# Kernel tuning notes

Hardware: AMD Instinct MI355X
Metric: run time of the kernel (lower is better)

Reference implementation:

```python
import jax, jax.numpy as jnp
import numpy as np

EPS = 1e-5

def setup_inputs() -> dict:
    key = jax.random.key(0)
    ks = jax.random.split(key, 8)
    N, D = 65536, 256
    x = jax.random.normal(ks[0], (N, D), dtype=jnp.float32)
    # BatchNorm1d affine params (frozen, torch default init)
    bn_gamma = jnp.ones((D,), jnp.float32)
    bn_beta = jnp.zeros((D,), jnp.float32)
    # Linear layers, torch default uniform(-1/sqrt(fan_in), 1/sqrt(fan_in))
    def lin(k, fin, fout):
        k1, k2 = jax.random.split(k)
        bound = 1.0 / np.sqrt(fin)
        W = jax.random.uniform(k1, (fout, fin), jnp.float32, -bound, bound)
        b = jax.random.uniform(k2, (fout,), jnp.float32, -bound, bound)
        return W, b
    W1, b1 = lin(ks[1], D, 512)
    W2, b2 = lin(ks[2], 512, 2048)
    Wf, bf = lin(ks[3], 2048, D)
    return {"x": x, "bn_gamma": bn_gamma, "bn_beta": bn_beta,
            "W1": W1, "b1": b1, "W2": W2, "b2": b2, "Wf": Wf, "bf": bf}


def reference(x, bn_gamma, bn_beta, W1, b1, W2, b2, Wf, bf):
    # BatchNorm1d in training mode: per-batch mean / biased variance
    mu = jnp.mean(x, axis=0)
    var = jnp.mean(jnp.square(x - mu), axis=0)
    xn = (x - mu) * jax.lax.rsqrt(var + EPS) * bn_gamma + bn_beta
    raw_feats = jnp.tanh(xn)
    h = xn @ W1.T + b1          # [N, 512]
    h = h @ W2.T + b2           # [N, 2048]
    out = jnp.tanh(h @ Wf.T + bf)  # [N, latent_dim]
    return (out, raw_feats)
```

## Files before the change

kernel.cpp:

```cpp
#include <hip/hip_runtime.h>
#include <hip/hip_bf16.h>
#include <stdint.h>

#define NROWS 65536
#define DFEAT 256

typedef __bf16 bf16x8 __attribute__((ext_vector_type(8)));
typedef float f32x4 __attribute__((ext_vector_type(4)));

__device__ __forceinline__ float fast_tanh(float x) {
    return 1.0f - 2.0f / (__expf(2.0f * x) + 1.0f);
}

__device__ __forceinline__ void gload_lds16(const void* g, void* l) {
    __builtin_amdgcn_global_load_lds(
        (const __attribute__((address_space(1))) unsigned int*)g,
        (__attribute__((address_space(3))) unsigned int*)l, 16, 0, 0);
}

__global__ void stats_kernel(const float4* __restrict__ x4,
                             float* __restrict__ sums,
                             float* __restrict__ sumsq) {
    __shared__ float ps[4][256];
    __shared__ float pq[4][256];
    int t = threadIdx.x;
    int c4 = t & 63;
    int r  = t >> 6;
    size_t i0 = (size_t)blockIdx.x * 128;
    float4 s = make_float4(0.f, 0.f, 0.f, 0.f);
    float4 q = make_float4(0.f, 0.f, 0.f, 0.f);
    for (int i = r; i < 128; i += 4) {
        float4 v = x4[(i0 + i) * 64 + c4];
        s.x += v.x; s.y += v.y; s.z += v.z; s.w += v.w;
        q.x += v.x * v.x; q.y += v.y * v.y; q.z += v.z * v.z; q.w += v.w * v.w;
    }
    ps[r][c4 * 4 + 0] = s.x; ps[r][c4 * 4 + 1] = s.y;
    ps[r][c4 * 4 + 2] = s.z; ps[r][c4 * 4 + 3] = s.w;
    pq[r][c4 * 4 + 0] = q.x; pq[r][c4 * 4 + 1] = q.y;
    pq[r][c4 * 4 + 2] = q.z; pq[r][c4 * 4 + 3] = q.w;
    __syncthreads();
    float ts = ps[0][t] + ps[1][t] + ps[2][t] + ps[3][t];
    float tq = pq[0][t] + pq[1][t] + pq[2][t] + pq[3][t];
    atomicAdd(&sums[t], ts);
    atomicAdd(&sumsq[t], tq);
}

__global__ void finalize_mvu_kernel(const float* __restrict__ sums,
                                    const float* __restrict__ sumsq,
                                    const float* __restrict__ gamma,
                                    const float* __restrict__ beta,
                                    float* __restrict__ scl,
                                    float* __restrict__ sft,
                                    const float* __restrict__ W2,
                                    const float* __restrict__ b1,
                                    const float* __restrict__ b2,
                                    float* __restrict__ u) {
    int t = threadIdx.x;
    if (blockIdx.x == 0) {
        const float invN = 1.0f / (float)NROWS;
        float mu  = sums[t] * invN;
        float var = sumsq[t] * invN - mu * mu;
        float rs  = rsqrtf(var + 1e-5f);
        float a   = gamma[t] * rs;
        scl[t] = a;
        sft[t] = beta[t] - mu * a;
        return;
    }
    int lane = t & 63;
    int row = (blockIdx.x - 1) * 4 + (t >> 6);
    const float* Wr = W2 + (size_t)row * 512;
    float s = 0.f;
    for (int k = lane; k < 512; k += 64) s += Wr[k] * b1[k];
    #pragma unroll
    for (int off = 32; off; off >>= 1) s += __shfl_xor(s, off);
    if (lane == 0) u[row] = s + b2[row];
}

__global__ void pgemm_kernel(const float* __restrict__ A,
                             const float* __restrict__ B,
                             float* __restrict__ C) {
    __shared__ float As[32][33];
    __shared__ float Bs[32][33];
    int t = threadIdx.x;
    int tx = t & 15, ty = t >> 4;
    int bi = blockIdx.y * 32;
    int bj = blockIdx.x * 32;
    int kb = blockIdx.z * 512;
    int row = t >> 3;
    int col = (t & 7) * 4;
    float acc00 = 0.f, acc01 = 0.f, acc10 = 0.f, acc11 = 0.f;
    for (int k0 = kb; k0 < kb + 512; k0 += 32) {
        float4 av = *(const float4*)&A[(size_t)(bi + row) * 2048 + k0 + col];
        As[row][col + 0] = av.x; As[row][col + 1] = av.y;
        As[row][col + 2] = av.z; As[row][col + 3] = av.w;
        float4 bv = *(const float4*)&B[(size_t)(k0 + row) * 512 + bj + col];
        Bs[row][col + 0] = bv.x; Bs[row][col + 1] = bv.y;
        Bs[row][col + 2] = bv.z; Bs[row][col + 3] = bv.w;
        __syncthreads();
        #pragma unroll
        for (int k = 0; k < 32; ++k) {
            float a0 = As[ty * 2 + 0][k];
            float a1 = As[ty * 2 + 1][k];
            float b0 = Bs[k][tx * 2 + 0];
            float b1v = Bs[k][tx * 2 + 1];
            acc00 += a0 * b0; acc01 += a0 * b1v;
            acc10 += a1 * b0; acc11 += a1 * b1v;
        }
        __syncthreads();
    }
    int i = bi + ty * 2, j = bj + tx * 2;
    atomicAdd(&C[(size_t)(i + 0) * 512 + j + 0], acc00);
    atomicAdd(&C[(size_t)(i + 0) * 512 + j + 1], acc01);
    atomicAdd(&C[(size_t)(i + 1) * 512 + j + 0], acc10);
    atomicAdd(&C[(size_t)(i + 1) * 512 + j + 1], acc11);
}

__global__ void collapse2_kernel(const float* __restrict__ P,
                                 const float* __restrict__ W1,
                                 const float* __restrict__ Wf,
                                 const float* __restrict__ u,
                                 const float* __restrict__ bfv,
                                 __bf16* __restrict__ Bprep,
                                 float* __restrict__ cv) {
    __shared__ float As[32][33];
    __shared__ float Bs[32][33];
    int t = threadIdx.x;
    if (blockIdx.x >= 64) {
        int lane = t & 63;
        int row = (blockIdx.x - 64) * 4 + (t >> 6);
        const float* Wr = Wf + (size_t)row * 2048;
        float s = 0.f;
        for (int k = lane; k < 2048; k += 64) s += Wr[k] * u[k];
        #pragma unroll
        for (int off = 32; off; off >>= 1) s += __shfl_xor(s, off);
        if (lane == 0) cv[row] = s + bfv[row];
        return;
    }
    int tx = t & 15, ty = t >> 4;
    int bi = (blockIdx.x >> 3) * 32;
    int bj = (blockIdx.x & 7) * 32;
    int row = t >> 3;
    int col = (t & 7) * 4;
    float acc00 = 0.f, acc01 = 0.f, acc10 = 0.f, acc11 = 0.f;
    for (int k0 = 0; k0 < 512; k0 += 32) {
        float4 av = *(const float4*)&P[(size_t)(bi + row) * 512 + k0 + col];
        As[row][col + 0] = av.x; As[row][col + 1] = av.y;
        As[row][col + 2] = av.z; As[row][col + 3] = av.w;
        float4 bv = *(const float4*)&W1[(size_t)(k0 + row) * 256 + bj + col];
        Bs[row][col + 0] = bv.x; Bs[row][col + 1] = bv.y;
        Bs[row][col + 2] = bv.z; Bs[row][col + 3] = bv.w;
        __syncthreads();
        #pragma unroll
        for (int k = 0; k < 32; ++k) {
            float a0 = As[ty * 2 + 0][k];
            float a1 = As[ty * 2 + 1][k];
            float b0 = Bs[k][tx * 2 + 0];
            float b1v = Bs[k][tx * 2 + 1];
            acc00 += a0 * b0; acc01 += a0 * b1v;
            acc10 += a1 * b0; acc11 += a1 * b1v;
        }
        __syncthreads();
    }
    int j = bi + ty * 2, k = bj + tx * 2;
    float vals[2][2] = {{acc00, acc01}, {acc10, acc11}};
    #pragma unroll
    for (int dj = 0; dj < 2; ++dj)
        #pragma unroll
        for (int dk = 0; dk < 2; ++dk) {
            float v = vals[dj][dk];
            int jj = j + dj, kk = k + dk;
            __bf16 h = (__bf16)v;
            __bf16 lo = (__bf16)(v - (float)h);
            int kstep = kk >> 5, kgrp = (kk >> 3) & 3, e = kk & 7;
            Bprep[((((size_t)kstep * 2 + 0) * 4 + kgrp) * 256 + jj) * 8 + e] = h;
            Bprep[((((size_t)kstep * 2 + 1) * 4 + kgrp) * 256 + jj) * 8 + e] = lo;
        }
}

__global__ __launch_bounds__(256)
void main_mfma(const float4* __restrict__ x4,
               const float* __restrict__ scl,
               const float* __restrict__ sft,
               const __bf16* __restrict__ Bprep,
               const float* __restrict__ cvec,
               float* __restrict__ out,
               float4* __restrict__ rf4) {
    __shared__ __align__(16) __bf16 Abuf[2][4][64][8];
    __shared__ __align__(16) __bf16 Bbuf[2][4][256][8];
    __shared__ float ss[256], sh[256];
    int t = threadIdx.x;
    int l = t & 63;
    int w = t >> 6;
    ss[t] = scl[t];
    sh[t] = sft[t];
    size_t row0 = (size_t)blockIdx.x * 64;
    int arow = t >> 2;
    int akg  = t & 3;

    f32x4 acc[4][4];
    #pragma unroll
    for (int i = 0; i < 4; ++i)
        #pragma unroll
        for (int j = 0; j < 4; ++j)
            acc[i][j] = (f32x4){0.f, 0.f, 0.f, 0.f};
    __syncthreads();

    int g = l >> 4, li = l & 15;
    for (int s = 0; s < 8; ++s) {
        const __bf16* bsrc = Bprep + (size_t)s * 16384;
        __bf16* bdst = &Bbuf[0][0][0][0];
        #pragma unroll
        for (int c = 0; c < 8; ++c) {
            int slot = c * 256 + t;
            gload_lds16(bsrc + (size_t)slot * 8, bdst + (size_t)slot * 8);
        }
        size_t xbase = (row0 + arow) * 64 + s * 8 + akg * 2;
        float4 v0 = x4[xbase];
        float4 v1 = x4[xbase + 1];
        int kb = s * 32 + akg * 8;
        float xn[8];
        xn[0] = v0.x * ss[kb + 0] + sh[kb + 0];
        xn[1] = v0.y * ss[kb + 1] + sh[kb + 1];
        xn[2] = v0.z * ss[kb + 2] + sh[kb + 2];
        xn[3] = v0.w * ss[kb + 3] + sh[kb + 3];
        xn[4] = v1.x * ss[kb + 4] + sh[kb + 4];
        xn[5] = v1.y * ss[kb + 5] + sh[kb + 5];
        xn[6] = v1.z * ss[kb + 6] + sh[kb + 6];
        xn[7] = v1.w * ss[kb + 7] + sh[kb + 7];
        float4 r0, r1;
        r0.x = fast_tanh(xn[0]); r0.y = fast_tanh(xn[1]);
        r0.z = fast_tanh(xn[2]); r0.w = fast_tanh(xn[3]);
        r1.x = fast_tanh(xn[4]); r1.y = fast_tanh(xn[5]);
        r1.z = fast_tanh(xn[6]); r1.w = fast_tanh(xn[7]);
        rf4[xbase] = r0;
        rf4[xbase + 1] = r1;
        bf16x8 hv, lv;
        #pragma unroll
        for (int e = 0; e < 8; ++e) {
            __bf16 h = (__bf16)xn[e];
            hv[e] = h;
            lv[e] = (__bf16)(xn[e] - (float)h);
        }
        int rx = arow ^ (akg << 1);
        *(bf16x8*)&Abuf[0][akg][rx][0] = hv;
        *(bf16x8*)&Abuf[1][akg][rx][0] = lv;
        __syncthreads();

        bf16x8 ah[4], al[4];
        #pragma unroll
        for (int i = 0; i < 4; ++i) {
            int rxr = (i * 16 + li) ^ (g << 1);
            ah[i] = *(const bf16x8*)&Abuf[0][g][rxr][0];
            al[i] = *(const bf16x8*)&Abuf[1][g][rxr][0];
        }
        #pragma unroll
        for (int j = 0; j < 4; ++j) {
            int coll = w * 64 + j * 16 + li;
            bf16x8 bh = *(const bf16x8*)&Bbuf[0][g][coll][0];
            bf16x8 bl = *(const bf16x8*)&Bbuf[1][g][coll][0];
            #pragma unroll
            for (int i = 0; i < 4; ++i) {
                acc[i][j] = __builtin_amdgcn_mfma_f32_16x16x32_bf16(ah[i], bh, acc[i][j], 0, 0, 0);
                acc[i][j] = __builtin_amdgcn_mfma_f32_16x16x32_bf16(al[i], bh, acc[i][j], 0, 0, 0);
                acc[i][j] = __builtin_amdgcn_mfma_f32_16x16x32_bf16(ah[i], bl, acc[i][j], 0, 0, 0);
            }
        }
        __syncthreads();
    }

    #pragma unroll
    for (int j = 0; j < 4; ++j) {
        int gcol = w * 64 + j * 16 + li;
        float cj = cvec[gcol];
        #pragma unroll
        for (int i = 0; i < 4; ++i) {
            #pragma unroll
            for (int r = 0; r < 4; ++r) {
                size_t grow = row0 + i * 16 + g * 4 + r;
                out[grow * 256 + gcol] = fast_tanh(acc[i][j][r] + cj);
            }
        }
    }
}

extern "C" void kernel_launch(void* const* d_in, const int* in_sizes, int n_in,
                              void* d_out, int out_size, void* d_ws, size_t ws_size,
                              hipStream_t stream) {
    const float* x     = (const float*)d_in[0];
    const float* gamma = (const float*)d_in[1];
    const float* beta  = (const float*)d_in[2];
    const float* W1    = (const float*)d_in[3];
    const float* b1    = (const float*)d_in[4];
    const float* W2    = (const float*)d_in[5];
    const float* b2    = (const float*)d_in[6];
    const float* Wf    = (const float*)d_in[7];
    const float* bf    = (const float*)d_in[8];

    float* out = (float*)d_out;
    float* rf  = out + (size_t)NROWS * DFEAT;

    float* ws    = (float*)d_ws;
    float* sums  = ws;
    float* sumsq = ws + 256;
    float* P     = ws + 512;
    float* u     = ws + 131584;
    float* cv    = ws + 133632;
    float* scl   = ws + 133888;
    float* sft   = ws + 134144;
    __bf16* Bprep = (__bf16*)(ws + 134400);

    hipMemsetAsync(ws, 0, (size_t)131584 * sizeof(float), stream);

    stats_kernel<<<512, 256, 0, stream>>>((const float4*)x, sums, sumsq);
    finalize_mvu_kernel<<<513, 256, 0, stream>>>(sums, sumsq, gamma, beta,
                                                 scl, sft, W2, b1, b2, u);
    pgemm_kernel<<<dim3(512 / 32, 256 / 32, 4), 256, 0, stream>>>(Wf, W2, P);
    collapse2_kernel<<<128, 256, 0, stream>>>(P, W1, Wf, u, bf, Bprep, cv);
    main_mfma<<<NROWS / 64, 256, 0, stream>>>((const float4*)x, scl, sft,
                                              Bprep, cv, out, (float4*)rf);
}
```

Baseline: 285.5 us.

## Merge prep kernels into two launches and read B fragments straight from global

Folds the batch-stats, W2·b1, and Wf·W2 partial GEMM into a single kernel that branches on block index, and merges the stats finalize into the collapse kernel, cutting the launch count from five to three. The main MFMA kernel no longer stages the bf16 weight tiles through LDS with global_load_lds. Each wave now loads its B fragments directly from global memory, and scale/shift are read as float4 from global, so most LDS traffic and one barrier go away. It also adds an occupancy hint of 4 blocks per CU and drops the XOR swizzle on the A buffer. The swizzle removal risks LDS bank conflicts, and the direct global B reads rely on cache hits.

```diff
diff --git a/kernel.cpp b/kernel.cpp
--- a/kernel.cpp
+++ b/kernel.cpp
@@ -12,51 +12,104 @@
     return 1.0f - 2.0f / (__expf(2.0f * x) + 1.0f);
 }
 
-__device__ __forceinline__ void gload_lds16(const void* g, void* l) {
-    __builtin_amdgcn_global_load_lds(
-        (const __attribute__((address_space(1))) unsigned int*)g,
-        (__attribute__((address_space(3))) unsigned int*)l, 16, 0, 0);
-}
-
-__global__ void stats_kernel(const float4* __restrict__ x4,
-                             float* __restrict__ sums,
-                             float* __restrict__ sumsq) {
-    __shared__ float ps[4][256];
-    __shared__ float pq[4][256];
+__global__ void k1_kernel(const float4* __restrict__ x4,
+                          float* __restrict__ sums,
+                          float* __restrict__ sumsq,
+                          const float* __restrict__ Wf,
+                          const float* __restrict__ W2,
+                          const float* __restrict__ b1,
+                          const float* __restrict__ b2,
+                          float* __restrict__ P,
+                          float* __restrict__ u) {
+    __shared__ float smem[2176];
     int t = threadIdx.x;
-    int c4 = t & 63;
-    int r  = t >> 6;
-    size_t i0 = (size_t)blockIdx.x * 128;
-    float4 s = make_float4(0.f, 0.f, 0.f, 0.f);
-    float4 q = make_float4(0.f, 0.f, 0.f, 0.f);
-    for (int i = r; i < 128; i += 4) {
-        float4 v = x4[(i0 + i) * 64 + c4];
-        s.x += v.x; s.y += v.y; s.z += v.z; s.w += v.w;
-        q.x += v.x * v.x; q.y += v.y * v.y; q.z += v.z * v.z; q.w += v.w * v.w;
-    }
-    ps[r][c4 * 4 + 0] = s.x; ps[r][c4 * 4 + 1] = s.y;
-    ps[r][c4 * 4 + 2] = s.z; ps[r][c4 * 4 + 3] = s.w;
-    pq[r][c4 * 4 + 0] = q.x; pq[r][c4 * 4 + 1] = q.y;
-    pq[r][c4 * 4 + 2] = q.z; pq[r][c4 * 4 + 3] = q.w;
-    __syncthreads();
-    float ts = ps[0][t] + ps[1][t] + ps[2][t] + ps[3][t];
-    float tq = pq[0][t] + pq[1][t] + pq[2][t] + pq[3][t];
-    atomicAdd(&sums[t], ts);
-    atomicAdd(&sumsq[t], tq);
-}
-
-__global__ void finalize_mvu_kernel(const float* __restrict__ sums,
-                                    const float* __restrict__ sumsq,
-                                    const float* __restrict__ gamma,
-                                    const float* __restrict__ beta,
-                                    float* __restrict__ scl,
-                                    float* __restrict__ sft,
-                                    const float* __restrict__ W2,
-                                    const float* __restrict__ b1,
-                                    const float* __restrict__ b2,
-                                    float* __restrict__ u) {
+    int b = blockIdx.x;
+    if (b < 512) {
+        float (*ps)[256] = (float (*)[256])smem;
+        float (*pq)[256] = (float (*)[256])(smem + 1024);
+        int c4 = t & 63;
+        int r  = t >> 6;
+        size_t i0 = (size_t)b * 128;
+        float4 s = make_float4(0.f, 0.f, 0.f, 0.f);
+        float4 q = make_float4(0.f, 0.f, 0.f, 0.f);
+        for (int i = r; i < 128; i += 4) {
+            float4 v = x4[(i0 + i) * 64 + c4];
+            s.x += v.x; s.y += v.y; s.z += v.z; s.w += v.w;
+            q.x += v.x * v.x; q.y += v.y * v.y; q.z += v.z * v.z; q.w += v.w * v.w;
+        }
+        ps[r][c4 * 4 + 0] = s.x; ps[r][c4 * 4 + 1] = s.y;
+        ps[r][c4 * 4 + 2] = s.z; ps[r][c4 * 4 + 3] = s.w;
+        pq[r][c4 * 4 + 0] = q.x; pq[r][c4 * 4 + 1] = q.y;
+        pq[r][c4 * 4 + 2] = q.z; pq[r][c4 * 4 + 3] = q.w;
+        __syncthreads();
+        float ts = ps[0][t] + ps[1][t] + ps[2][t] + ps[3][t];
+        float tq = pq[0][t] + pq[1][t] + pq[2][t] + pq[3][t];
+        atomicAdd(&sums[t], ts);
+        atomicAdd(&sumsq[t], tq);
+    } else if (b < 1024) {
+        int bb = b - 512;
+        int bj = (bb & 15) * 32;
+        int bi = ((bb >> 4) & 7) * 32;
+        int kb = (bb >> 7) * 512;
+        float (*As)[33] = (float (*)[33])smem;
+        float (*Bs)[33] = (float (*)[33])(smem + 1056);
+        int tx = t & 15, ty = t >> 4;
+        int row = t >> 3;
+        int col = (t & 7) * 4;
+        float acc00 = 0.f, acc01 = 0.f, acc10 = 0.f, acc11 = 0.f;
+        for (int k0 = kb; k0 < kb + 512; k0 += 32) {
+            float4 av = *(const float4*)&Wf[(size_t)(bi + row) * 2048 + k0 + col];
+            As[row][col + 0] = av.x; As[row][col + 1] = av.y;
+            As[row][col + 2] = av.z; As[row][col + 3] = av.w;
+            float4 bv = *(const float4*)&W2[(size_t)(k0 + row) * 512 + bj + col];
+            Bs[row][col + 0] = bv.x; Bs[row][col + 1] = bv.y;
+            Bs[row][col + 2] = bv.z; Bs[row][col + 3] = bv.w;
+            __syncthreads();
+            #pragma unroll
+            for (int k = 0; k < 32; ++k) {
+                float a0 = As[ty * 2 + 0][k];
+                float a1 = As[ty * 2 + 1][k];
+                float b0 = Bs[k][tx * 2 + 0];
+                float b1v = Bs[k][tx * 2 + 1];
+                acc00 += a0 * b0; acc01 += a0 * b1v;
+                acc10 += a1 * b0; acc11 += a1 * b1v;
+            }
+            __syncthreads();
+        }
+        int i = bi + ty * 2, j = bj + tx * 2;
+        atomicAdd(&P[(size_t)(i + 0) * 512 + j + 0], acc00);
+        atomicAdd(&P[(size_t)(i + 0) * 512 + j + 1], acc01);
+        atomicAdd(&P[(size_t)(i + 1) * 512 + j + 0], acc10);
+        atomicAdd(&P[(size_t)(i + 1) * 512 + j + 1], acc11);
+    } else {
+        int lane = t & 63;
+        int row = (b - 1024) * 4 + (t >> 6);
+        const float* Wr = W2 + (size_t)row * 512;
+        float s = 0.f;
+        for (int k = lane; k < 512; k += 64) s += Wr[k] * b1[k];
+        #pragma unroll
+        for (int off = 32; off; off >>= 1) s += __shfl_xor(s, off);
+        if (lane == 0) u[row] = s + b2[row];
+    }
+}
+
+__global__ void k2_kernel(const float* __restrict__ sums,
+                          const float* __restrict__ sumsq,
+                          const float* __restrict__ gamma,
+                          const float* __restrict__ beta,
+                          float* __restrict__ scl,
+                          float* __restrict__ sft,
+                          const float* __restrict__ P,
+                          const float* __restrict__ W1,
+                          const float* __restrict__ Wf,
+                          const float* __restrict__ u,
+                          const float* __restrict__ bfv,
+                          __bf16* __restrict__ Bprep,
+                          float* __restrict__ cv) {
+    __shared__ float smem[2176];
     int t = threadIdx.x;
-    if (blockIdx.x == 0) {
+    int b = blockIdx.x;
+    if (b >= 128) {
         const float invN = 1.0f / (float)NROWS;
         float mu  = sums[t] * invN;
         float var = sumsq[t] * invN - mu * mu;
@@ -66,68 +119,9 @@
         sft[t] = beta[t] - mu * a;
         return;
     }
-    int lane = t & 63;
-    int row = (blockIdx.x - 1) * 4 + (t >> 6);
-    const float* Wr = W2 + (size_t)row * 512;
-    float s = 0.f;
-    for (int k = lane; k < 512; k += 64) s += Wr[k] * b1[k];
-    #pragma unroll
-    for (int off = 32; off; off >>= 1) s += __shfl_xor(s, off);
-    if (lane == 0) u[row] = s + b2[row];
-}
-
-__global__ void pgemm_kernel(const float* __restrict__ A,
-                             const float* __restrict__ B,
-                             float* __restrict__ C) {
-    __shared__ float As[32][33];
-    __shared__ float Bs[32][33];
-    int t = threadIdx.x;
-    int tx = t & 15, ty = t >> 4;
-    int bi = blockIdx.y * 32;
-    int bj = blockIdx.x * 32;
-    int kb = blockIdx.z * 512;
-    int row = t >> 3;
-    int col = (t & 7) * 4;
-    float acc00 = 0.f, acc01 = 0.f, acc10 = 0.f, acc11 = 0.f;
-    for (int k0 = kb; k0 < kb + 512; k0 += 32) {
-        float4 av = *(const float4*)&A[(size_t)(bi + row) * 2048 + k0 + col];
-        As[row][col + 0] = av.x; As[row][col + 1] = av.y;
-        As[row][col + 2] = av.z; As[row][col + 3] = av.w;
-        float4 bv = *(const float4*)&B[(size_t)(k0 + row) * 512 + bj + col];
-        Bs[row][col + 0] = bv.x; Bs[row][col + 1] = bv.y;
-        Bs[row][col + 2] = bv.z; Bs[row][col + 3] = bv.w;
-        __syncthreads();
-        #pragma unroll
-        for (int k = 0; k < 32; ++k) {
-            float a0 = As[ty * 2 + 0][k];
-            float a1 = As[ty * 2 + 1][k];
-            float b0 = Bs[k][tx * 2 + 0];
-            float b1v = Bs[k][tx * 2 + 1];
-            acc00 += a0 * b0; acc01 += a0 * b1v;
-            acc10 += a1 * b0; acc11 += a1 * b1v;
-        }
-        __syncthreads();
-    }
-    int i = bi + ty * 2, j = bj + tx * 2;
-    atomicAdd(&C[(size_t)(i + 0) * 512 + j + 0], acc00);
-    atomicAdd(&C[(size_t)(i + 0) * 512 + j + 1], acc01);
-    atomicAdd(&C[(size_t)(i + 1) * 512 + j + 0], acc10);
-    atomicAdd(&C[(size_t)(i + 1) * 512 + j + 1], acc11);
-}
-
-__global__ void collapse2_kernel(const float* __restrict__ P,
-                                 const float* __restrict__ W1,
-                                 const float* __restrict__ Wf,
-                                 const float* __restrict__ u,
-                                 const float* __restrict__ bfv,
-                                 __bf16* __restrict__ Bprep,
-                                 float* __restrict__ cv) {
-    __shared__ float As[32][33];
-    __shared__ float Bs[32][33];
-    int t = threadIdx.x;
-    if (blockIdx.x >= 64) {
+    if (b >= 64) {
         int lane = t & 63;
-        int row = (blockIdx.x - 64) * 4 + (t >> 6);
+        int row = (b - 64) * 4 + (t >> 6);
         const float* Wr = Wf + (size_t)row * 2048;
         float s = 0.f;
         for (int k = lane; k < 2048; k += 64) s += Wr[k] * u[k];
@@ -136,9 +130,11 @@
         if (lane == 0) cv[row] = s + bfv[row];
         return;
     }
+    float (*As)[33] = (float (*)[33])smem;
+    float (*Bs)[33] = (float (*)[33])(smem + 1056);
     int tx = t & 15, ty = t >> 4;
-    int bi = (blockIdx.x >> 3) * 32;
-    int bj = (blockIdx.x & 7) * 32;
+    int bi = (b >> 3) * 32;
+    int bj = (b & 7) * 32;
     int row = t >> 3;
     int col = (t & 7) * 4;
     float acc00 = 0.f, acc01 = 0.f, acc10 = 0.f, acc11 = 0.f;
@@ -177,22 +173,19 @@
         }
 }
 
-__global__ __launch_bounds__(256)
+__global__ __launch_bounds__(256, 4)
 void main_mfma(const float4* __restrict__ x4,
-               const float* __restrict__ scl,
-               const float* __restrict__ sft,
+               const float4* __restrict__ scl4,
+               const float4* __restrict__ sft4,
                const __bf16* __restrict__ Bprep,
                const float* __restrict__ cvec,
                float* __restrict__ out,
                float4* __restrict__ rf4) {
-    __shared__ __align__(16) __bf16 Abuf[2][4][64][8];
-    __shared__ __align__(16) __bf16 Bbuf[2][4][256][8];
-    __shared__ float ss[256], sh[256];
+    __shared__ __align__(16) __bf16 Abuf[2][64][4][8];
     int t = threadIdx.x;
     int l = t & 63;
     int w = t >> 6;
-    ss[t] = scl[t];
-    sh[t] = sft[t];
+    int g = l >> 4, li = l & 15;
     size_t row0 = (size_t)blockIdx.x * 64;
     int arow = t >> 2;
     int akg  = t & 3;
@@ -203,30 +196,23 @@
         #pragma unroll
         for (int j = 0; j < 4; ++j)
             acc[i][j] = (f32x4){0.f, 0.f, 0.f, 0.f};
-    __syncthreads();
-
-    int g = l >> 4, li = l & 15;
+
     for (int s = 0; s < 8; ++s) {
-        const __bf16* bsrc = Bprep + (size_t)s * 16384;
-        __bf16* bdst = &Bbuf[0][0][0][0];
-        #pragma unroll
-        for (int c = 0; c < 8; ++c) {
-            int slot = c * 256 + t;
-            gload_lds16(bsrc + (size_t)slot * 8, bdst + (size_t)slot * 8);
-        }
         size_t xbase = (row0 + arow) * 64 + s * 8 + akg * 2;
         float4 v0 = x4[xbase];
         float4 v1 = x4[xbase + 1];
-        int kb = s * 32 + akg * 8;
+        int kb4 = s * 8 + akg * 2;
+        float4 sc0 = scl4[kb4], sc1 = scl4[kb4 + 1];
+        float4 sf0 = sft4[kb4], sf1 = sft4[kb4 + 1];
         float xn[8];
-        xn[0] = v0.x * ss[kb + 0] + sh[kb + 0];
-        xn[1] = v0.y * ss[kb + 1] + sh[kb + 1];
-        xn[2] = v0.z * ss[kb + 2] + sh[kb + 2];
-        xn[3] = v0.w * ss[kb + 3] + sh[kb + 3];
-        xn[4] = v1.x * ss[kb + 4] + sh[kb + 4];
-        xn[5] = v1.y * ss[kb + 5] + sh[kb + 5];
-        xn[6] = v1.z * ss[kb + 6] + sh[kb + 6];
-        xn[7] = v1.w * ss[kb + 7] + sh[kb + 7];
+        xn[0] = v0.x * sc0.x + sf0.x;
+        xn[1] = v0.y * sc0.y + sf0.y;
+        xn[2] = v0.z * sc0.z + sf0.z;
+        xn[3] = v0.w * sc0.w + sf0.w;
+        xn[4] = v1.x * sc1.x + sf1.x;
+        xn[5] = v1.y * sc1.y + sf1.y;
+        xn[6] = v1.z * sc1.z + sf1.z;
+        xn[7] = v1.w * sc1.w + sf1.w;
         float4 r0, r1;
         r0.x = fast_tanh(xn[0]); r0.y = fast_tanh(xn[1]);
         r0.z = fast_tanh(xn[2]); r0.w = fast_tanh(xn[3]);
@@ -241,23 +227,23 @@
             hv[e] = h;
             lv[e] = (__bf16)(xn[e] - (float)h);
         }
-        int rx = arow ^ (akg << 1);
-        *(bf16x8*)&Abuf[0][akg][rx][0] = hv;
-        *(bf16x8*)&Abuf[1][akg][rx][0] = lv;
+        *(bf16x8*)&Abuf[0][arow][akg][0] = hv;
+        *(bf16x8*)&Abuf[1][arow][akg][0] = lv;
         __syncthreads();
 
         bf16x8 ah[4], al[4];
         #pragma unroll
         for (int i = 0; i < 4; ++i) {
-            int rxr = (i * 16 + li) ^ (g << 1);
-            ah[i] = *(const bf16x8*)&Abuf[0][g][rxr][0];
-            al[i] = *(const bf16x8*)&Abuf[1][g][rxr][0];
-        }
+            ah[i] = *(const bf16x8*)&Abuf[0][i * 16 + li][g][0];
+            al[i] = *(const bf16x8*)&Abuf[1][i * 16 + li][g][0];
+        }
+        const __bf16* bh_base = Bprep + (size_t)(8 * s + g) * 2048;
+        const __bf16* bl_base = Bprep + (size_t)(8 * s + 4 + g) * 2048;
         #pragma unroll
         for (int j = 0; j < 4; ++j) {
             int coll = w * 64 + j * 16 + li;
-            bf16x8 bh = *(const bf16x8*)&Bbuf[0][g][coll][0];
-            bf16x8 bl = *(const bf16x8*)&Bbuf[1][g][coll][0];
+            bf16x8 bh = *(const bf16x8*)&bh_base[(size_t)coll * 8];
+            bf16x8 bl = *(const bf16x8*)&bl_base[(size_t)coll * 8];
             #pragma unroll
             for (int i = 0; i < 4; ++i) {
                 acc[i][j] = __builtin_amdgcn_mfma_f32_16x16x32_bf16(ah[i], bh, acc[i][j], 0, 0, 0);
@@ -311,11 +297,12 @@
 
     hipMemsetAsync(ws, 0, (size_t)131584 * sizeof(float), stream);
 
-    stats_kernel<<<512, 256, 0, stream>>>((const float4*)x, sums, sumsq);
-    finalize_mvu_kernel<<<513, 256, 0, stream>>>(sums, sumsq, gamma, beta,
-                                                 scl, sft, W2, b1, b2, u);
-    pgemm_kernel<<<dim3(512 / 32, 256 / 32, 4), 256, 0, stream>>>(Wf, W2, P);
-    collapse2_kernel<<<128, 256, 0, stream>>>(P, W1, Wf, u, bf, Bprep, cv);
-    main_mfma<<<NROWS / 64, 256, 0, stream>>>((const float4*)x, scl, sft,
+    k1_kernel<<<1536, 256, 0, stream>>>((const float4*)x, sums, sumsq,
+                                        Wf, W2, b1, b2, P, u);
+    k2_kernel<<<129, 256, 0, stream>>>(sums, sumsq, gamma, beta, scl, sft,
+                                       P, W1, Wf, u, bf, Bprep, cv);
+    main_mfma<<<NROWS / 64, 256, 0, stream>>>((const float4*)x,
+                                              (const float4*)scl,
+                                              (const float4*)sft,
                                               Bprep, cv, out, (float4*)rf);
 }
```

Result: faster. 258.5 us (-9.4%).
